# Optimization experiments

Hardware: AMD Instinct MI355X
Metric: run time of the kernel (lower is better)

## Reference

```python
import jax, jax.numpy as jnp
import numpy as np

NV, NE = 2048, 8192
IN_V, OUT_V, IN_E = 128, 128, 128


def setup_inputs() -> dict:
    key = jax.random.key(0)
    ks = jax.random.split(key, 8)
    stdv = 1.0 / np.sqrt(OUT_V)
    return {
        "H_v": jax.random.normal(ks[0], (NV, IN_V), jnp.float32),
        "H_e": jax.random.normal(ks[1], (NE, IN_E), jnp.float32),
        "adj_e": jax.random.uniform(ks[2], (NE, NE), jnp.float32),
        "adj_v": jax.random.uniform(ks[3], (NV, NV), jnp.float32),
        "T": jax.random.uniform(ks[4], (NV, NE), jnp.float32),
        "weight": jax.random.uniform(ks[5], (IN_V, OUT_V), jnp.float32, -stdv, stdv),
        "p": jax.random.normal(ks[6], (1, IN_E), jnp.float32),
        "bias": jax.random.uniform(ks[7], (OUT_V,), jnp.float32, -stdv, stdv),
    }


def reference(H_v, H_e, adj_e, adj_v, T, weight, p, bias):
    # node_layer=True branch.
    # edge scalar weights: diag(H_e @ p^T) -> just a vector of length NE
    w = (H_e @ p.T)[:, 0]                      # [NE]
    # T @ diag(w) @ T^T == (T * w) @ T^T  (column-scale then GEMM)
    multiplier1 = (T * w[None, :]) @ T.T       # [NV, NV]
    eye = jnp.eye(multiplier1.shape[0], dtype=multiplier1.dtype)
    M1 = eye + (1.0 - eye) * multiplier1       # ones on diag, multiplier1 off-diag
    adjusted_A = M1 * adj_v                    # masked adjacency
    ret = adjusted_A @ (H_v @ weight) + bias   # [NV, OUT_V]
    return (ret, H_e)
```

## Files before the change

### kernel.cpp

```cpp
#include <hip/hip_runtime.h>
#include <hip/hip_bf16.h>
#include <stdint.h>
#include <stddef.h>

#define NV 2048
#define NE 8192
#define KSPLIT 8
#define KCHUNK (NE / KSPLIT)

typedef __bf16 bf16_t;
typedef __bf16 bf16x4 __attribute__((ext_vector_type(4)));
typedef __bf16 bf16x8 __attribute__((ext_vector_type(8)));
typedef float f32x4 __attribute__((ext_vector_type(4)));

__device__ static inline void load_lds16(const void* g, void* lds) {
  __builtin_amdgcn_global_load_lds(
      (const __attribute__((address_space(1))) void*)g,
      (__attribute__((address_space(3))) void*)lds,
      16, 0, 0);
}

__device__ static inline void tile_decode(int tile, int& bi, int& bj) {
  int b = (int)((sqrtf(8.f * tile + 1.f) - 1.f) * 0.5f);
  while ((b + 1) * (b + 2) / 2 <= tile) b++;
  while (b * (b + 1) / 2 > tile) b--;
  bi = b;
  bj = tile - b * (b + 1) / 2;
}

__global__ void k_w(const float* __restrict__ He, const float* __restrict__ p,
                    float* __restrict__ w) {
  int wave = threadIdx.x >> 6;
  int lane = threadIdx.x & 63;
  int e = blockIdx.x * 4 + wave;
  float v = He[(size_t)e * 128 + lane] * p[lane]
          + He[(size_t)e * 128 + 64 + lane] * p[64 + lane];
#pragma unroll
  for (int off = 32; off > 0; off >>= 1) v += __shfl_down(v, off, 64);
  if (lane == 0) w[e] = v;
}

__global__ void k_conv(const float* __restrict__ T, const float* __restrict__ w,
                       bf16_t* __restrict__ A, bf16_t* __restrict__ B) {
  size_t idx = (size_t)blockIdx.x * 256 + threadIdx.x;
  size_t base = idx * 4;
  int col = (int)(base & (NE - 1));
  f32x4 t = *(const f32x4*)(T + base);
  f32x4 w4 = *(const f32x4*)(w + col);
  bf16x4 a, b;
  a.x = (bf16_t)(t.x * w4.x); a.y = (bf16_t)(t.y * w4.y);
  a.z = (bf16_t)(t.z * w4.z); a.w = (bf16_t)(t.w * w4.w);
  b.x = (bf16_t)t.x; b.y = (bf16_t)t.y; b.z = (bf16_t)t.z; b.w = (bf16_t)t.w;
  *(bf16x4*)(A + base) = a;
  *(bf16x4*)(B + base) = b;
}

__global__ void k_hw(const float* __restrict__ Hv, const float* __restrict__ Wt,
                     bf16_t* __restrict__ HWt) {
  int t = blockIdx.x * 256 + threadIdx.x;
  int o = t & 127, j = t >> 7;
  const float* hv = Hv + (size_t)j * 128;
  float acc = 0.f;
#pragma unroll 4
  for (int k = 0; k < 128; ++k) acc += hv[k] * Wt[k * 128 + o];
  HWt[(size_t)o * NV + j] = (bf16_t)acc;
}

__global__ void k_gemm1(const bf16_t* __restrict__ A, const bf16_t* __restrict__ B,
                        float* __restrict__ P) {
  __shared__ bf16_t As[128 * 64];
  __shared__ bf16_t Bs[128 * 64];
  const int t = threadIdx.x;
  const int lane = t & 63;
  const int wv = t >> 6;
  const int wm = wv >> 1, wn = wv & 1;

  int bi, bj;
  tile_decode(blockIdx.x, bi, bj);
  const int i0 = bi * 128, j0 = bj * 128;
  const int kbeg = blockIdx.y * KCHUNK;
  float* Mp = P + (size_t)blockIdx.y * NV * NV;

  f32x4 acc[4][4] = {};

  const int lrow = t >> 3;
  const int lcol = (t & 7) * 8;
  const bf16_t* Ag = A + (size_t)(i0 + lrow) * NE + lcol;
  const bf16_t* Bg = B + (size_t)(j0 + lrow) * NE + lcol;

  for (int k0 = kbeg; k0 < kbeg + KCHUNK; k0 += 64) {
    __syncthreads();
#pragma unroll
    for (int it = 0; it < 4; ++it) {
      load_lds16(Ag + (size_t)(it * 32) * NE + k0, (char*)As + (it * 256 + t) * 16);
      load_lds16(Bg + (size_t)(it * 32) * NE + k0, (char*)Bs + (it * 256 + t) * 16);
    }
    __syncthreads();
#pragma unroll
    for (int kk = 0; kk < 64; kk += 32) {
      bf16x8 af[4], bfr[4];
#pragma unroll
      for (int mt = 0; mt < 4; ++mt)
        af[mt] = *(const bf16x8*)&As[(wm * 64 + mt * 16 + (lane & 15)) * 64 + kk + (lane >> 4) * 8];
#pragma unroll
      for (int nt = 0; nt < 4; ++nt)
        bfr[nt] = *(const bf16x8*)&Bs[(wn * 64 + nt * 16 + (lane & 15)) * 64 + kk + (lane >> 4) * 8];
#pragma unroll
      for (int mt = 0; mt < 4; ++mt)
#pragma unroll
        for (int nt = 0; nt < 4; ++nt)
          acc[mt][nt] = __builtin_amdgcn_mfma_f32_16x16x32_bf16(af[mt], bfr[nt], acc[mt][nt], 0, 0, 0);
    }
  }

#pragma unroll
  for (int mt = 0; mt < 4; ++mt) {
#pragma unroll
    for (int nt = 0; nt < 4; ++nt) {
      int gc = j0 + wn * 64 + nt * 16 + (lane & 15);
#pragma unroll
      for (int r = 0; r < 4; ++r) {
        int gr = i0 + wm * 64 + mt * 16 + (lane >> 4) * 4 + r;
        Mp[(size_t)gr * NV + gc] = acc[mt][nt][r];
      }
    }
  }
}

__global__ void k_mask(const float* __restrict__ P, const float* __restrict__ adj_v,
                       bf16_t* __restrict__ adjA) {
  __shared__ float Ms[128 * 129];
  const int t = threadIdx.x;
  int bi, bj;
  tile_decode(blockIdx.x, bi, bj);
  const int i0 = bi * 128, j0 = bj * 128;
  const bool diag = (bi == bj);
#pragma unroll 2
  for (int c = 0; c < 64; ++c) {
    int e = c * 256 + t;
    int r = e >> 7, col = e & 127;
    size_t gidx = (size_t)(i0 + r) * NV + j0 + col;
    float v = 0.f;
#pragma unroll
    for (int s = 0; s < KSPLIT; ++s) v += P[(size_t)s * NV * NV + gidx];
    float vv = (diag && r == col) ? 1.0f : v;
    adjA[gidx] = (bf16_t)(vv * adj_v[gidx]);
    if (!diag) Ms[col * 129 + r] = v;
  }
  if (diag) return;
  __syncthreads();
#pragma unroll 2
  for (int c = 0; c < 64; ++c) {
    int e = c * 256 + t;
    int r = e >> 7, col = e & 127;
    size_t gidx = (size_t)(j0 + r) * NV + i0 + col;
    adjA[gidx] = (bf16_t)(Ms[r * 129 + col] * adj_v[gidx]);
  }
}

__global__ void k_gemm2(const bf16_t* __restrict__ adjA, const bf16_t* __restrict__ HWt,
                        const float* __restrict__ bias, float* __restrict__ out) {
  __shared__ bf16_t As[128 * 64];
  __shared__ bf16_t Bs[128 * 64];
  const int t = threadIdx.x;
  const int lane = t & 63;
  const int wv = t >> 6;
  const int wm = wv >> 1, wn = wv & 1;
  const int i0 = blockIdx.x * 128;

  f32x4 acc[4][4] = {};

  const int lrow = t >> 3;
  const int lcol = (t & 7) * 8;
  const bf16_t* Ag = adjA + (size_t)(i0 + lrow) * NV + lcol;
  const bf16_t* Bg = HWt + (size_t)lrow * NV + lcol;

  for (int k0 = 0; k0 < NV; k0 += 64) {
    __syncthreads();
#pragma unroll
    for (int it = 0; it < 4; ++it) {
      load_lds16(Ag + (size_t)(it * 32) * NV + k0, (char*)As + (it * 256 + t) * 16);
      load_lds16(Bg + (size_t)(it * 32) * NV + k0, (char*)Bs + (it * 256 + t) * 16);
    }
    __syncthreads();
#pragma unroll
    for (int kk = 0; kk < 64; kk += 32) {
      bf16x8 af[4], bfr[4];
#pragma unroll
      for (int mt = 0; mt < 4; ++mt)
        af[mt] = *(const bf16x8*)&As[(wm * 64 + mt * 16 + (lane & 15)) * 64 + kk + (lane >> 4) * 8];
#pragma unroll
      for (int nt = 0; nt < 4; ++nt)
        bfr[nt] = *(const bf16x8*)&Bs[(wn * 64 + nt * 16 + (lane & 15)) * 64 + kk + (lane >> 4) * 8];
#pragma unroll
      for (int mt = 0; mt < 4; ++mt)
#pragma unroll
        for (int nt = 0; nt < 4; ++nt)
          acc[mt][nt] = __builtin_amdgcn_mfma_f32_16x16x32_bf16(af[mt], bfr[nt], acc[mt][nt], 0, 0, 0);
    }
  }

#pragma unroll
  for (int mt = 0; mt < 4; ++mt) {
#pragma unroll
    for (int nt = 0; nt < 4; ++nt) {
      int gc = wn * 64 + nt * 16 + (lane & 15);
      float bo = bias[gc];
#pragma unroll
      for (int r = 0; r < 4; ++r) {
        int gr = i0 + wm * 64 + mt * 16 + (lane >> 4) * 4 + r;
        out[(size_t)gr * 128 + gc] = acc[mt][nt][r] + bo;
      }
    }
  }
}

extern "C" void kernel_launch(void* const* d_in, const int* in_sizes, int n_in,
                              void* d_out, int out_size, void* d_ws, size_t ws_size,
                              hipStream_t stream) {
  const float* Hv     = (const float*)d_in[0];
  const float* He     = (const float*)d_in[1];
  const float* adj_v  = (const float*)d_in[3];
  const float* T      = (const float*)d_in[4];
  const float* weight = (const float*)d_in[5];
  const float* p      = (const float*)d_in[6];
  const float* bias   = (const float*)d_in[7];
  float* out = (float*)d_out;

  char* ws = (char*)d_ws;
  bf16_t* A_bf  = (bf16_t*)ws;
  bf16_t* B_bf  = (bf16_t*)(ws + 33554432);
  float*  P     = (float*)(ws + 67108864);
  bf16_t* adjAb = (bf16_t*)(ws + 201326592);
  bf16_t* HWt   = (bf16_t*)(ws + 209715200);
  float*  w     = (float*)(ws + 210239488);

  k_w<<<NE / 4, 256, 0, stream>>>(He, p, w);
  k_conv<<<(NV * NE / 4) / 256, 256, 0, stream>>>(T, w, A_bf, B_bf);
  k_hw<<<(NV * 128) / 256, 256, 0, stream>>>(Hv, weight, HWt);
  dim3 g1(136, KSPLIT);
  k_gemm1<<<g1, 256, 0, stream>>>(A_bf, B_bf, P);
  k_mask<<<136, 256, 0, stream>>>(P, adj_v, adjAb);
  k_gemm2<<<NV / 128, 256, 0, stream>>>(adjAb, HWt, bias, out);
  hipMemcpyAsync(out + (size_t)NV * 128, He, (size_t)NE * 128 * sizeof(float),
                 hipMemcpyDeviceToDevice, stream);
}
```

Measured before the change: 536.1 us.

## Store split-K partials as bf16 tiles, swizzle LDS, split-K second GEMM

The first GEMM now writes its split-K partials as contiguous bf16 128x128 tiles instead of full fp32 NVxNV slabs, which cuts partial-sum traffic into the mask kernel. The mask kernel reads them with 8-wide vector loads. Both GEMMs gain an XOR-style rotation of the LDS layout to avoid bank conflicts. The second GEMM is split 8-way along K to use more CUs, with a new reduction kernel that adds the bias. Storing partials in bf16 loses some precision before the sum, and the extra launch plus fp32 partials add some overhead.

```diff
diff --git a/kernel.cpp b/kernel.cpp
--- a/kernel.cpp
+++ b/kernel.cpp
@@ -67,7 +67,7 @@
 }
 
 __global__ void k_gemm1(const bf16_t* __restrict__ A, const bf16_t* __restrict__ B,
-                        float* __restrict__ P) {
+                        bf16_t* __restrict__ P) {
   __shared__ bf16_t As[128 * 64];
   __shared__ bf16_t Bs[128 * 64];
   const int t = threadIdx.x;
@@ -79,14 +79,14 @@
   tile_decode(blockIdx.x, bi, bj);
   const int i0 = bi * 128, j0 = bj * 128;
   const int kbeg = blockIdx.y * KCHUNK;
-  float* Mp = P + (size_t)blockIdx.y * NV * NV;
+  bf16_t* Mp = P + ((size_t)blockIdx.x * KSPLIT + blockIdx.y) * 16384;
 
   f32x4 acc[4][4] = {};
 
   const int lrow = t >> 3;
-  const int lcol = (t & 7) * 8;
-  const bf16_t* Ag = A + (size_t)(i0 + lrow) * NE + lcol;
-  const bf16_t* Bg = B + (size_t)(j0 + lrow) * NE + lcol;
+  const int cb = ((t & 7) + lrow) & 7;
+  const bf16_t* Ag = A + (size_t)(i0 + lrow) * NE + cb * 8;
+  const bf16_t* Bg = B + (size_t)(j0 + lrow) * NE + cb * 8;
 
   for (int k0 = kbeg; k0 < kbeg + KCHUNK; k0 += 64) {
     __syncthreads();
@@ -100,11 +100,17 @@
     for (int kk = 0; kk < 64; kk += 32) {
       bf16x8 af[4], bfr[4];
 #pragma unroll
-      for (int mt = 0; mt < 4; ++mt)
-        af[mt] = *(const bf16x8*)&As[(wm * 64 + mt * 16 + (lane & 15)) * 64 + kk + (lane >> 4) * 8];
-#pragma unroll
-      for (int nt = 0; nt < 4; ++nt)
-        bfr[nt] = *(const bf16x8*)&Bs[(wn * 64 + nt * 16 + (lane & 15)) * 64 + kk + (lane >> 4) * 8];
+      for (int mt = 0; mt < 4; ++mt) {
+        int row = wm * 64 + mt * 16 + (lane & 15);
+        int sw = (((kk >> 3) + (lane >> 4)) - row) & 7;
+        af[mt] = *(const bf16x8*)&As[row * 64 + sw * 8];
+      }
+#pragma unroll
+      for (int nt = 0; nt < 4; ++nt) {
+        int row = wn * 64 + nt * 16 + (lane & 15);
+        int sw = (((kk >> 3) + (lane >> 4)) - row) & 7;
+        bfr[nt] = *(const bf16x8*)&Bs[row * 64 + sw * 8];
+      }
 #pragma unroll
       for (int mt = 0; mt < 4; ++mt)
 #pragma unroll
@@ -117,17 +123,17 @@
   for (int mt = 0; mt < 4; ++mt) {
 #pragma unroll
     for (int nt = 0; nt < 4; ++nt) {
-      int gc = j0 + wn * 64 + nt * 16 + (lane & 15);
+      int tc = wn * 64 + nt * 16 + (lane & 15);
 #pragma unroll
       for (int r = 0; r < 4; ++r) {
-        int gr = i0 + wm * 64 + mt * 16 + (lane >> 4) * 4 + r;
-        Mp[(size_t)gr * NV + gc] = acc[mt][nt][r];
-      }
-    }
-  }
-}
-
-__global__ void k_mask(const float* __restrict__ P, const float* __restrict__ adj_v,
+        int tr = wm * 64 + mt * 16 + (lane >> 4) * 4 + r;
+        Mp[tr * 128 + tc] = (bf16_t)acc[mt][nt][r];
+      }
+    }
+  }
+}
+
+__global__ void k_mask(const bf16_t* __restrict__ P, const float* __restrict__ adj_v,
                        bf16_t* __restrict__ adjA) {
   __shared__ float Ms[128 * 129];
   const int t = threadIdx.x;
@@ -135,31 +141,52 @@
   tile_decode(blockIdx.x, bi, bj);
   const int i0 = bi * 128, j0 = bj * 128;
   const bool diag = (bi == bj);
+  const bf16_t* Pt = P + (size_t)blockIdx.x * (KSPLIT * 16384);
 #pragma unroll 2
-  for (int c = 0; c < 64; ++c) {
-    int e = c * 256 + t;
-    int r = e >> 7, col = e & 127;
-    size_t gidx = (size_t)(i0 + r) * NV + j0 + col;
-    float v = 0.f;
-#pragma unroll
-    for (int s = 0; s < KSPLIT; ++s) v += P[(size_t)s * NV * NV + gidx];
-    float vv = (diag && r == col) ? 1.0f : v;
-    adjA[gidx] = (bf16_t)(vv * adj_v[gidx]);
-    if (!diag) Ms[col * 129 + r] = v;
+  for (int c = 0; c < 8; ++c) {
+    int e0 = (c * 256 + t) * 8;
+    int r = e0 >> 7, col = e0 & 127;
+    float v[8] = {};
+#pragma unroll
+    for (int s = 0; s < KSPLIT; ++s) {
+      bf16x8 pv = *(const bf16x8*)(Pt + s * 16384 + e0);
+#pragma unroll
+      for (int u = 0; u < 8; ++u) v[u] += (float)pv[u];
+    }
+    size_t g = (size_t)(i0 + r) * NV + j0 + col;
+    f32x4 av0 = *(const f32x4*)(adj_v + g);
+    f32x4 av1 = *(const f32x4*)(adj_v + g + 4);
+    bf16x8 outv;
+#pragma unroll
+    for (int u = 0; u < 8; ++u) {
+      float vv = (diag && r == col + u) ? 1.0f : v[u];
+      outv[u] = (bf16_t)(vv * (u < 4 ? av0[u] : av1[u - 4]));
+    }
+    *(bf16x8*)(adjA + g) = outv;
+    if (!diag) {
+#pragma unroll
+      for (int u = 0; u < 8; ++u) Ms[(col + u) * 129 + r] = v[u];
+    }
   }
   if (diag) return;
   __syncthreads();
 #pragma unroll 2
-  for (int c = 0; c < 64; ++c) {
-    int e = c * 256 + t;
-    int r = e >> 7, col = e & 127;
-    size_t gidx = (size_t)(j0 + r) * NV + i0 + col;
-    adjA[gidx] = (bf16_t)(Ms[r * 129 + col] * adj_v[gidx]);
+  for (int c = 0; c < 8; ++c) {
+    int e0 = (c * 256 + t) * 8;
+    int r = e0 >> 7, col = e0 & 127;
+    size_t g = (size_t)(j0 + r) * NV + i0 + col;
+    f32x4 av0 = *(const f32x4*)(adj_v + g);
+    f32x4 av1 = *(const f32x4*)(adj_v + g + 4);
+    bf16x8 outv;
+#pragma unroll
+    for (int u = 0; u < 8; ++u)
+      outv[u] = (bf16_t)(Ms[r * 129 + col + u] * (u < 4 ? av0[u] : av1[u - 4]));
+    *(bf16x8*)(adjA + g) = outv;
   }
 }
 
 __global__ void k_gemm2(const bf16_t* __restrict__ adjA, const bf16_t* __restrict__ HWt,
-                        const float* __restrict__ bias, float* __restrict__ out) {
+                        float* __restrict__ P2) {
   __shared__ bf16_t As[128 * 64];
   __shared__ bf16_t Bs[128 * 64];
   const int t = threadIdx.x;
@@ -167,15 +194,17 @@
   const int wv = t >> 6;
   const int wm = wv >> 1, wn = wv & 1;
   const int i0 = blockIdx.x * 128;
+  const int kbeg = blockIdx.y * 256;
+  float* Pp = P2 + (size_t)blockIdx.y * (NV * 128);
 
   f32x4 acc[4][4] = {};
 
   const int lrow = t >> 3;
-  const int lcol = (t & 7) * 8;
-  const bf16_t* Ag = adjA + (size_t)(i0 + lrow) * NV + lcol;
-  const bf16_t* Bg = HWt + (size_t)lrow * NV + lcol;
-
-  for (int k0 = 0; k0 < NV; k0 += 64) {
+  const int cb = ((t & 7) + lrow) & 7;
+  const bf16_t* Ag = adjA + (size_t)(i0 + lrow) * NV + cb * 8;
+  const bf16_t* Bg = HWt + (size_t)lrow * NV + cb * 8;
+
+  for (int k0 = kbeg; k0 < kbeg + 256; k0 += 64) {
     __syncthreads();
 #pragma unroll
     for (int it = 0; it < 4; ++it) {
@@ -187,11 +216,17 @@
     for (int kk = 0; kk < 64; kk += 32) {
       bf16x8 af[4], bfr[4];
 #pragma unroll
-      for (int mt = 0; mt < 4; ++mt)
-        af[mt] = *(const bf16x8*)&As[(wm * 64 + mt * 16 + (lane & 15)) * 64 + kk + (lane >> 4) * 8];
-#pragma unroll
-      for (int nt = 0; nt < 4; ++nt)
-        bfr[nt] = *(const bf16x8*)&Bs[(wn * 64 + nt * 16 + (lane & 15)) * 64 + kk + (lane >> 4) * 8];
+      for (int mt = 0; mt < 4; ++mt) {
+        int row = wm * 64 + mt * 16 + (lane & 15);
+        int sw = (((kk >> 3) + (lane >> 4)) - row) & 7;
+        af[mt] = *(const bf16x8*)&As[row * 64 + sw * 8];
+      }
+#pragma unroll
+      for (int nt = 0; nt < 4; ++nt) {
+        int row = wn * 64 + nt * 16 + (lane & 15);
+        int sw = (((kk >> 3) + (lane >> 4)) - row) & 7;
+        bfr[nt] = *(const bf16x8*)&Bs[row * 64 + sw * 8];
+      }
 #pragma unroll
       for (int mt = 0; mt < 4; ++mt)
 #pragma unroll
@@ -205,14 +240,23 @@
 #pragma unroll
     for (int nt = 0; nt < 4; ++nt) {
       int gc = wn * 64 + nt * 16 + (lane & 15);
-      float bo = bias[gc];
 #pragma unroll
       for (int r = 0; r < 4; ++r) {
         int gr = i0 + wm * 64 + mt * 16 + (lane >> 4) * 4 + r;
-        out[(size_t)gr * 128 + gc] = acc[mt][nt][r] + bo;
-      }
-    }
-  }
+        Pp[(size_t)gr * 128 + gc] = acc[mt][nt][r];
+      }
+    }
+  }
+}
+
+__global__ void k_bias(const float* __restrict__ P2, const float* __restrict__ bias,
+                       float* __restrict__ out) {
+  int idx = (blockIdx.x * 256 + threadIdx.x) * 4;
+  f32x4 acc = {};
+#pragma unroll
+  for (int s = 0; s < 8; ++s) acc += *(const f32x4*)(P2 + (size_t)s * NV * 128 + idx);
+  f32x4 b = *(const f32x4*)(bias + (idx & 127));
+  *(f32x4*)(out + idx) = acc + b;
 }
 
 extern "C" void kernel_launch(void* const* d_in, const int* in_sizes, int n_in,
@@ -230,18 +274,21 @@
   char* ws = (char*)d_ws;
   bf16_t* A_bf  = (bf16_t*)ws;
   bf16_t* B_bf  = (bf16_t*)(ws + 33554432);
-  float*  P     = (float*)(ws + 67108864);
-  bf16_t* adjAb = (bf16_t*)(ws + 201326592);
-  bf16_t* HWt   = (bf16_t*)(ws + 209715200);
-  float*  w     = (float*)(ws + 210239488);
+  bf16_t* P1    = (bf16_t*)(ws + 67108864);
+  bf16_t* adjAb = (bf16_t*)(ws + 104857600);
+  float*  P2    = (float*)(ws + 113246208);
+  bf16_t* HWt   = (bf16_t*)(ws + 121634816);
+  float*  w     = (float*)(ws + 122155008);
 
   k_w<<<NE / 4, 256, 0, stream>>>(He, p, w);
   k_conv<<<(NV * NE / 4) / 256, 256, 0, stream>>>(T, w, A_bf, B_bf);
   k_hw<<<(NV * 128) / 256, 256, 0, stream>>>(Hv, weight, HWt);
   dim3 g1(136, KSPLIT);
-  k_gemm1<<<g1, 256, 0, stream>>>(A_bf, B_bf, P);
-  k_mask<<<136, 256, 0, stream>>>(P, adj_v, adjAb);
-  k_gemm2<<<NV / 128, 256, 0, stream>>>(adjAb, HWt, bias, out);
+  k_gemm1<<<g1, 256, 0, stream>>>(A_bf, B_bf, P1);
+  k_mask<<<136, 256, 0, stream>>>(P1, adj_v, adjAb);
+  dim3 g2(NV / 128, 8);
+  k_gemm2<<<g2, 256, 0, stream>>>(adjAb, HWt, P2);
+  k_bias<<<NV * 128 / 4 / 256, 256, 0, stream>>>(P2, bias, out);
   hipMemcpyAsync(out + (size_t)NV * 128, He, (size_t)NE * 128 * sizeof(float),
                  hipMemcpyDeviceToDevice, stream);
 }
```

Measured after the change: 477.3 us. 1.12x faster.
